# Performance work log

Hardware: AMD Instinct MI355X
Metric: run time of the kernel (lower is better)

## Reference

```python
import jax, jax.numpy as jnp
import numpy as np

B, D, C = 512, 512, 100000
M1, M2, M3 = 1.0, 0.5, 0.0  # canonical ArcFace margins
EPS = 1e-12  # tf.nn.l2_normalize epsilon


def _l2norm(v, axis):
    return v * jax.lax.rsqrt(jnp.maximum(jnp.sum(v * v, axis=axis, keepdims=True), EPS))


def setup_inputs() -> dict:
    key = jax.random.key(0)
    k1, k2, k3 = jax.random.split(key, 3)
    x = jax.random.normal(k1, (B, D), dtype=jnp.float32)
    W = jax.random.normal(k2, (D, C), dtype=jnp.float32)
    label_idx = jax.random.randint(k3, (B,), 0, C, dtype=jnp.int32)
    return {"x": x, "W": W, "label_idx": label_idx}


def reference(x, W, label_idx):
    xn = _l2norm(x, axis=1)            # [B, D] unit embeddings
    Wn = _l2norm(W, axis=0)            # [D, C] unit class weights (norm=True fc)
    logits = xn @ Wn                   # [B, C] cosine similarities
    # gather target cosine per row (gather_nd over one-hot label)
    t = jnp.take_along_axis(logits, label_idx[:, None], axis=1)[:, 0]  # [B]
    # m1 == 1.0 -> skip angular scaling branch; m2 != 0 -> additive angular margin
    t = jnp.arccos(t) + M2
    # clamp to pi value-wise, straight-through gradient: t1 = t + pi - stop_grad(t)
    t = jnp.minimum(t, t + (jnp.pi - jax.lax.stop_gradient(t)))
    t = jnp.cos(t)
    onehot = jax.nn.one_hot(label_idx, C, dtype=logits.dtype)  # [B, C]
    out = logits * (1.0 - onehot) + t[:, None] * onehot
    out = out - onehot * M3
    return out
```

## Files before the change

kernel.cpp:

```cpp
#include <hip/hip_runtime.h>
#include <math.h>

#define BB 512
#define DD 512
#define CC 100000
#define MARGIN2 0.5f
#define PI_F 3.14159265358979323846f

#define BM 128
#define BN 128
#define BK 64
#define KSTEPS (DD / BK)
#define NPAN 782
#define GRID (4 * NPAN)

typedef __bf16 bf16x8 __attribute__((ext_vector_type(8)));
typedef float f32x4 __attribute__((ext_vector_type(4)));

static __device__ __forceinline__ unsigned short f2bf(float f) {
    union { float f; unsigned u; } v; v.f = f;
    unsigned r = v.u + 0x7FFFu + ((v.u >> 16) & 1u);
    return (unsigned short)(r >> 16);
}

static __device__ __forceinline__ int swz(int row, int kbyte) {
    return row * 128 + (kbyte ^ ((row & 7) << 4));
}

static __device__ __forceinline__ void gll16(const unsigned char* g, unsigned char* l) {
    __builtin_amdgcn_global_load_lds(
        (const __attribute__((address_space(1))) void*)g,
        (__attribute__((address_space(3))) void*)l, 16, 0, 0);
}

__global__ __launch_bounds__(256) void k_norm_x(const float* __restrict__ x,
                                                unsigned char* __restrict__ img) {
    const int lane = threadIdx.x & 63;
    const int row  = blockIdx.x * 4 + (threadIdx.x >> 6);
    const float* xr = x + (size_t)row * DD;
    float4 v0 = *(const float4*)(xr + lane * 4);
    float4 v1 = *(const float4*)(xr + lane * 4 + 256);
    float s = v0.x*v0.x + v0.y*v0.y + v0.z*v0.z + v0.w*v0.w
            + v1.x*v1.x + v1.y*v1.y + v1.z*v1.z + v1.w*v1.w;
    #pragma unroll
    for (int m = 32; m; m >>= 1) s += __shfl_xor(s, m, 64);
    float rs = rsqrtf(fmaxf(s, 1e-12f));
    ushort4 o0, o1;
    o0.x = f2bf(v0.x * rs); o0.y = f2bf(v0.y * rs);
    o0.z = f2bf(v0.z * rs); o0.w = f2bf(v0.w * rs);
    o1.x = f2bf(v1.x * rs); o1.y = f2bf(v1.y * rs);
    o1.z = f2bf(v1.z * rs); o1.w = f2bf(v1.w * rs);

    const int mb   = row >> 7;
    const int lrow = row & 127;
    const int k0   = lane * 4;
    const int t0   = k0 >> 6;
    const int c8   = (k0 >> 3) & 7;
    const int sub  = (k0 >> 2) & 1;
    const int base = (mb * 8 + t0) * 16384 + lrow * 128
                   + ((c8 * 16) ^ ((lrow & 7) << 4)) + sub * 8;
    *(ushort4*)(img + base)         = o0;
    *(ushort4*)(img + base + 65536) = o1;
}

#define ABUF 16384
#define LDSZ (2 * ABUF + 2 * 16384 + 512)

__global__ __launch_bounds__(512, 4) void k_gemm(const unsigned char* __restrict__ img,
                                                 const float* __restrict__ W,
                                                 float* __restrict__ out) {
    __shared__ __align__(16) unsigned char LDS[LDSZ];
    unsigned char* bufA = LDS;
    unsigned char* bufB = LDS + 2 * ABUF;
    float* rn = (float*)(LDS + 2 * ABUF + 32768);

    const int tid = threadIdx.x;
    const int bid = blockIdx.x;

    const int v  = (bid & 7) * 391 + (bid >> 3);
    const int mb = v & 3;
    const int nb = v >> 2;
    const int M0 = mb * BM;
    const int N0 = nb * BN;

    const int lane = tid & 63;
    const int wid  = tid >> 6;
    const int wm = wid >> 2;
    const int wn = wid & 3;
    const int lr = lane & 15;
    const int lg = lane >> 4;

    int b_go[4], b_ld[4];
    #pragma unroll
    for (int i = 0; i < 4; ++i) {
        int s  = tid + i * 512;
        int n  = s & 127;
        int kq = s >> 7;
        int col = N0 + n;
        col = col < CC ? col : CC - 1;
        b_go[i] = kq * 4 * CC + col;
        b_ld[i] = n * 128 + ((kq * 8) ^ ((n & 7) << 4));
    }

    const unsigned char* imgA = img + mb * (8 * ABUF);
    const int lds_u = wid * 2048;

    float f0[4][4], f1[4][4];
    float bsq[4] = {0.f, 0.f, 0.f, 0.f};

#define WAITV_(N) asm volatile("s_waitcnt vmcnt(" #N ")" ::: "memory")
#define WAITV(N) WAITV_(N)
#define SB() __builtin_amdgcn_sched_barrier(0)

#define LOAD_B(FR, T) do {                                                     \
    _Pragma("unroll")                                                          \
    for (int i = 0; i < 4; ++i) {                                              \
        const float* p = W + b_go[i] + (size_t)(T) * (BK * CC);                \
        FR[i][0] = p[0];      FR[i][1] = p[CC];                                \
        FR[i][2] = p[2 * CC]; FR[i][3] = p[3 * CC];                            \
    } } while (0)

#define PACK_WRITE(FR, T) do {                                                 \
    unsigned char* dst = bufB + ((T) & 1) * 16384;                             \
    _Pragma("unroll")                                                          \
    for (int i = 0; i < 4; ++i) {                                              \
        bsq[i] += FR[i][0] * FR[i][0] + FR[i][1] * FR[i][1]                    \
                + FR[i][2] * FR[i][2] + FR[i][3] * FR[i][3];                   \
        unsigned w0, w1;                                                       \
        asm("v_cvt_pk_bf16_f32 %0, %1, %2" : "=v"(w0) : "v"(FR[i][0]), "v"(FR[i][1])); \
        asm("v_cvt_pk_bf16_f32 %0, %1, %2" : "=v"(w1) : "v"(FR[i][2]), "v"(FR[i][3])); \
        uint2 w; w.x = w0; w.y = w1;                                           \
        *(uint2*)(dst + b_ld[i]) = w;                                          \
    } } while (0)

#define GLL_A(T) do {                                                          \
    unsigned char* A_nxt = bufA + ((T) & 1) * ABUF;                            \
    const unsigned char* gsrc = imgA + (T) * ABUF;                             \
    gll16(gsrc + lds_u + lane * 16, A_nxt + lds_u);                            \
    gll16(gsrc + lds_u + 1024 + lane * 16, A_nxt + lds_u + 1024);              \
    } while (0)

#define COMPUTE(T) do {                                                        \
    const unsigned char* A_cur = bufA + ((T) & 1) * ABUF;                      \
    const unsigned char* B_cur = bufB + ((T) & 1) * 16384;                     \
    __builtin_amdgcn_s_setprio(1);                                             \
    _Pragma("unroll")                                                          \
    for (int ks = 0; ks < 2; ++ks) {                                           \
        bf16x8 af[4], bfr[2];                                                  \
        _Pragma("unroll")                                                      \
        for (int mf = 0; mf < 4; ++mf)                                         \
            af[mf] = *(const bf16x8*)(A_cur + swz(wm * 64 + mf * 16 + lr, ks * 64 + lg * 16)); \
        _Pragma("unroll")                                                      \
        for (int nf = 0; nf < 2; ++nf)                                         \
            bfr[nf] = *(const bf16x8*)(B_cur + swz(wn * 32 + nf * 16 + lr, ks * 64 + lg * 16)); \
        _Pragma("unroll")                                                      \
        for (int mf = 0; mf < 4; ++mf)                                         \
            _Pragma("unroll")                                                  \
            for (int nf = 0; nf < 2; ++nf)                                     \
                acc[mf][nf] = __builtin_amdgcn_mfma_f32_16x16x32_bf16(         \
                    bfr[nf], af[mf], acc[mf][nf], 0, 0, 0);                    \
    }                                                                          \
    __builtin_amdgcn_s_setprio(0);                                             \
    } while (0)

#define KBODY(T, FP, FN) do {                                                  \
    if ((T) + 1 < KSTEPS) GLL_A((T) + 1);                                      \
    SB();                                                                      \
    COMPUTE(T);                                                                \
    SB();                                                                      \
    if ((T) + 1 < KSTEPS) PACK_WRITE(FP, (T) + 1);                             \
    if ((T) + 2 < KSTEPS) LOAD_B(FN, (T) + 2);                                 \
    SB();                                                                      \
    if ((T) + 1 < KSTEPS) {                                                    \
        if ((T) + 2 < KSTEPS) { WAITV(16); } else { WAITV(0); }                \
        SB();                                                                  \
        asm volatile("s_waitcnt lgkmcnt(0)" ::: "memory"); SB();               \
        __builtin_amdgcn_s_barrier(); SB();                                    \
    } } while (0)

    f32x4 acc[4][2];
    #pragma unroll
    for (int mf = 0; mf < 4; ++mf)
        #pragma unroll
        for (int nf = 0; nf < 2; ++nf)
            acc[mf][nf] = (f32x4)0.f;

    LOAD_B(f0, 0);
    GLL_A(0);
    SB();
    PACK_WRITE(f0, 0);
    LOAD_B(f1, 1);
    SB();
    WAITV(16); SB();
    asm volatile("s_waitcnt lgkmcnt(0)" ::: "memory"); SB();
    __builtin_amdgcn_s_barrier(); SB();

    KBODY(0, f1, f0);
    KBODY(1, f0, f1);
    KBODY(2, f1, f0);
    KBODY(3, f0, f1);
    KBODY(4, f1, f0);
    KBODY(5, f0, f1);
    KBODY(6, f1, f0);
    KBODY(7, f0, f1);

    __syncthreads();
    float* part = (float*)bufB;
    #pragma unroll
    for (int i = 0; i < 4; ++i)
        part[tid + i * 512] = bsq[i];
    __syncthreads();
    if (tid < BN) {
        float s = 0.f;
        #pragma unroll
        for (int k = 0; k < 16; ++k)
            s += part[k * BN + tid];
        rn[tid] = rsqrtf(fmaxf(s, 1e-12f));
    }
    __syncthreads();

    float* stag = (float*)bufA;
    #pragma unroll
    for (int rd = 0; rd < 4; ++rd) {
        if (wm == (rd >> 1)) {
            #pragma unroll
            for (int f = 0; f < 2; ++f) {
                const int mf = (rd & 1) * 2 + f;
                const int ml = f * 16 + lr;
                #pragma unroll
                for (int nf = 0; nf < 2; ++nf) {
                    const int nl = wn * 32 + nf * 16 + lg * 4;
                    const f32x4 rn4 = *(const f32x4*)(rn + nl);
                    f32x4 o;
                    #pragma unroll
                    for (int r = 0; r < 4; ++r)
                        o[r] = acc[mf][nf][r] * rn4[r];
                    *(f32x4*)(stag + ml * 132 + nl) = o;
                }
            }
        }
        __syncthreads();
        #pragma unroll
        for (int j = tid; j < 1024; j += 512) {
            const int m = j >> 5;
            const int n = (j & 31) * 4;
            if (N0 + n + 4 <= CC) {
                f32x4 o = *(const f32x4*)(stag + m * 132 + n);
                __builtin_nontemporal_store(o,
                    (f32x4*)(out + (size_t)(M0 + rd * 32 + m) * CC + N0 + n));
            }
        }
        __syncthreads();
    }
}

__global__ __launch_bounds__(512) void k_fix(const int* __restrict__ lab,
                                             float* __restrict__ out) {
    const int b = threadIdx.x;
    const int c = lab[b];
    const size_t idx = (size_t)b * CC + c;
    float t = out[idx];
    t = fminf(fmaxf(t, -1.f), 1.f);
    float th = acosf(t) + MARGIN2;
    th = fminf(th, PI_F);
    out[idx] = cosf(th);
}

extern "C" void kernel_launch(void* const* d_in, const int* in_sizes, int n_in,
                              void* d_out, int out_size, void* d_ws, size_t ws_size,
                              hipStream_t stream) {
    const float* x   = (const float*)d_in[0];
    const float* W   = (const float*)d_in[1];
    const int*   lab = (const int*)d_in[2];
    float* out = (float*)d_out;

    unsigned char* img = (unsigned char*)d_ws;

    k_norm_x<<<dim3(BB / 4), dim3(256), 0, stream>>>(x, img);
    k_gemm<<<dim3(GRID), dim3(512), 0, stream>>>(img, W, out);
    k_fix<<<dim3(1), dim3(512), 0, stream>>>(lab, out);
}
```

Measured before the change: 110.3 us.

## Deepen W prefetch to three register buffers with 8-row-per-thread loads

Restructures the W-tile loading so each thread loads 8 consecutive k-rows for 2 columns instead of 4 rows for 4 columns. This lets each thread write a 16-byte bf16 chunk to LDS in a single store. It also adds a third register buffer so global loads for W run two k-steps ahead instead of one, to hide more HBM latency for the streamed W matrix. The cost is more VGPRs held live, which may reduce occupancy. The per-column norm reduction now sums 8 partials instead of 16.

New measurement: 112.1 us. Within noise of the previous version (+1.7%).

```diff
diff --git a/kernel.cpp b/kernel.cpp
--- a/kernel.cpp
+++ b/kernel.cpp
@@ -90,23 +90,23 @@
     const int lr = lane & 15;
     const int lg = lane >> 4;
 
-    int b_go[4], b_ld[4];
-    #pragma unroll
-    for (int i = 0; i < 4; ++i) {
+    int b_go[2], b_ld[2];
+    #pragma unroll
+    for (int i = 0; i < 2; ++i) {
         int s  = tid + i * 512;
         int n  = s & 127;
-        int kq = s >> 7;
+        int o  = s >> 7;
         int col = N0 + n;
         col = col < CC ? col : CC - 1;
-        b_go[i] = kq * 4 * CC + col;
-        b_ld[i] = n * 128 + ((kq * 8) ^ ((n & 7) << 4));
+        b_go[i] = o * 8 * CC + col;
+        b_ld[i] = n * 128 + ((o * 16) ^ ((n & 7) << 4));
     }
 
     const unsigned char* imgA = img + mb * (8 * ABUF);
     const int lds_u = wid * 2048;
 
-    float f0[4][4], f1[4][4];
-    float bsq[4] = {0.f, 0.f, 0.f, 0.f};
+    float f0[2][8], f1[2][8], f2[2][8];
+    float bsq[2] = {0.f, 0.f};
 
 #define WAITV_(N) asm volatile("s_waitcnt vmcnt(" #N ")" ::: "memory")
 #define WAITV(N) WAITV_(N)
@@ -114,23 +114,26 @@
 
 #define LOAD_B(FR, T) do {                                                     \
     _Pragma("unroll")                                                          \
-    for (int i = 0; i < 4; ++i) {                                              \
+    for (int i = 0; i < 2; ++i) {                                              \
         const float* p = W + b_go[i] + (size_t)(T) * (BK * CC);                \
-        FR[i][0] = p[0];      FR[i][1] = p[CC];                                \
-        FR[i][2] = p[2 * CC]; FR[i][3] = p[3 * CC];                            \
+        _Pragma("unroll")                                                      \
+        for (int j = 0; j < 8; ++j)                                            \
+            FR[i][j] = p[(size_t)j * CC];                                      \
     } } while (0)
 
 #define PACK_WRITE(FR, T) do {                                                 \
     unsigned char* dst = bufB + ((T) & 1) * 16384;                             \
     _Pragma("unroll")                                                          \
-    for (int i = 0; i < 4; ++i) {                                              \
-        bsq[i] += FR[i][0] * FR[i][0] + FR[i][1] * FR[i][1]                    \
-                + FR[i][2] * FR[i][2] + FR[i][3] * FR[i][3];                   \
-        unsigned w0, w1;                                                       \
-        asm("v_cvt_pk_bf16_f32 %0, %1, %2" : "=v"(w0) : "v"(FR[i][0]), "v"(FR[i][1])); \
-        asm("v_cvt_pk_bf16_f32 %0, %1, %2" : "=v"(w1) : "v"(FR[i][2]), "v"(FR[i][3])); \
-        uint2 w; w.x = w0; w.y = w1;                                           \
-        *(uint2*)(dst + b_ld[i]) = w;                                          \
+    for (int i = 0; i < 2; ++i) {                                              \
+        _Pragma("unroll")                                                      \
+        for (int j = 0; j < 8; ++j)                                            \
+            bsq[i] += FR[i][j] * FR[i][j];                                     \
+        uint4 w;                                                               \
+        asm("v_cvt_pk_bf16_f32 %0, %1, %2" : "=v"(w.x) : "v"(FR[i][0]), "v"(FR[i][1])); \
+        asm("v_cvt_pk_bf16_f32 %0, %1, %2" : "=v"(w.y) : "v"(FR[i][2]), "v"(FR[i][3])); \
+        asm("v_cvt_pk_bf16_f32 %0, %1, %2" : "=v"(w.z) : "v"(FR[i][4]), "v"(FR[i][5])); \
+        asm("v_cvt_pk_bf16_f32 %0, %1, %2" : "=v"(w.w) : "v"(FR[i][6]), "v"(FR[i][7])); \
+        *(uint4*)(dst + b_ld[i]) = w;                                          \
     } } while (0)
 
 #define GLL_A(T) do {                                                          \
@@ -169,10 +172,10 @@
     COMPUTE(T);                                                                \
     SB();                                                                      \
     if ((T) + 1 < KSTEPS) PACK_WRITE(FP, (T) + 1);                             \
-    if ((T) + 2 < KSTEPS) LOAD_B(FN, (T) + 2);                                 \
+    if ((T) + 3 < KSTEPS) LOAD_B(FN, (T) + 3);                                 \
     SB();                                                                      \
     if ((T) + 1 < KSTEPS) {                                                    \
-        if ((T) + 2 < KSTEPS) { WAITV(16); } else { WAITV(0); }                \
+        if ((T) + 3 < KSTEPS) { WAITV(16); } else { WAITV(0); }                \
         SB();                                                                  \
         asm volatile("s_waitcnt lgkmcnt(0)" ::: "memory"); SB();               \
         __builtin_amdgcn_s_barrier(); SB();                                    \
@@ -187,34 +190,35 @@
 
     LOAD_B(f0, 0);
     GLL_A(0);
+    LOAD_B(f1, 1);
     SB();
     PACK_WRITE(f0, 0);
-    LOAD_B(f1, 1);
+    LOAD_B(f2, 2);
     SB();
-    WAITV(16); SB();
+    WAITV(32); SB();
     asm volatile("s_waitcnt lgkmcnt(0)" ::: "memory"); SB();
     __builtin_amdgcn_s_barrier(); SB();
 
     KBODY(0, f1, f0);
-    KBODY(1, f0, f1);
-    KBODY(2, f1, f0);
-    KBODY(3, f0, f1);
-    KBODY(4, f1, f0);
-    KBODY(5, f0, f1);
+    KBODY(1, f2, f1);
+    KBODY(2, f0, f2);
+    KBODY(3, f1, f0);
+    KBODY(4, f2, f1);
+    KBODY(5, f0, f2);
     KBODY(6, f1, f0);
-    KBODY(7, f0, f1);
+    KBODY(7, f2, f1);
 
     __syncthreads();
     float* part = (float*)bufB;
     #pragma unroll
-    for (int i = 0; i < 4; ++i)
+    for (int i = 0; i < 2; ++i)
         part[tid + i * 512] = bsq[i];
     __syncthreads();
     if (tid < BN) {
         float s = 0.f;
         #pragma unroll
-        for (int k = 0; k < 16; ++k)
-            s += part[k * BN + tid];
+        for (int o = 0; o < 8; ++o)
+            s += part[o * BN + tid];
         rn[tid] = rsqrtf(fmaxf(s, 1e-12f));
     }
     __syncthreads();
```
